# Kernel tuning notes

Measured on AMD Instinct MI355X. Metric: run time of the kernel, lower is better.

The kernel has to match this reference:

```python
import math
import jax, jax.numpy as jnp
import numpy as np

DIM = 256
B, S = 4, 4096

def setup_inputs() -> dict:
    key = jax.random.key(0)
    k1, k2, k3, k4 = jax.random.split(key, 4)
    x = jax.random.normal(k1, (B, S, DIM), dtype=jnp.float32)
    W = jax.random.normal(k2, (3 * DIM, DIM), dtype=jnp.float32) * 0.02
    b = jax.random.normal(k3, (3 * DIM,), dtype=jnp.float32) * 0.02
    attention_mask = jax.random.randint(k4, (B, 1, S), 0, 2, dtype=jnp.int32)
    return {"x": x, "W": W, "b": b, "attention_mask": attention_mask}

def reference(x, W, b, attention_mask):
    # qkv projection: Linear(dim, 3*dim) -> x @ W^T + b
    qkv = jnp.einsum("bsd,ed->bse", x, W) + b  # [B,S,3*DIM]
    q, k, v = jnp.split(qkv, 3, axis=-1)
    # NOTE: module computes q @ v^T (not q @ k^T) -- faithful to source
    scores = jnp.einsum("bqd,bkd->bqk", q, v) / math.sqrt(DIM)  # [B,S,S]
    scores = jnp.where(attention_mask == 0, -jnp.inf, scores)
    attn = jax.nn.softmax(scores, axis=-1)
    # dropout in eval mode -> identity
    out = jnp.einsum("bqk,bkd->bqd", attn, v)  # [B,S,DIM]
    return out
```

## Files before the change

kernel.cpp:

```cpp
#include <hip/hip_runtime.h>
#include <hip/hip_bf16.h>

#define DIMC 256
#define NB 4
#define NS 4096
#define KT 64
#define VS_ELEMS (KT * DIMC)

typedef __attribute__((ext_vector_type(4))) float f32x4;
typedef __attribute__((ext_vector_type(8))) short bf16x8;

__device__ __forceinline__ ushort f2bf(float f) {
  __hip_bfloat16 h = __float2bfloat16(f);
  return *reinterpret_cast<ushort*>(&h);
}
__device__ __forceinline__ float bf2f(ushort h) {
  uint u = ((uint)h) << 16;
  float f;
  __builtin_memcpy(&f, &u, 4);
  return f;
}

__device__ __forceinline__ void gload16(const ushort* g, ushort* l) {
  __builtin_amdgcn_global_load_lds(
      (const __attribute__((address_space(1))) unsigned int*)g,
      (__attribute__((address_space(3))) unsigned int*)l,
      16, 0, 0);
}

__global__ __launch_bounds__(256) void prep_kernel(
    const float* __restrict__ W, const int* __restrict__ mask,
    const float* __restrict__ x,
    ushort* __restrict__ Whl, uint* __restrict__ pm32,
    ushort* __restrict__ xhb, ushort* __restrict__ xlb)
{
  const int bid = blockIdx.x;
  if (bid < 512) {
    const int col = bid;
    const int k = threadIdx.x;
    const int srcrow = (col < 256) ? col : (col + 256);
    float f = W[(size_t)srcrow * 256 + k];
    ushort h = f2bf(f);
    Whl[(size_t)col * 256 + k] = h;
    Whl[131072 + (size_t)col * 256 + k] = f2bf(f - bf2f(h));
  } else if (bid < 514) {
    int t = (bid - 512) * 256 + threadIdx.x;
    int b = t >> 7;
    int kt = (t >> 1) & 63;
    int kh = t & 1;
    const int* mrow = mask + b * NS + kt * 64 + kh * 32;
    uint wd = 0;
    for (int g = 0; g < 4; ++g)
      for (int ntl = 0; ntl < 2; ++ntl)
        for (int r = 0; r < 4; ++r)
          if (mrow[ntl * 16 + 4 * g + r] != 0) wd |= 1u << (8 * g + ntl * 4 + r);
    pm32[t] = wd;
  } else {
    size_t idx = ((size_t)(bid - 514) * 256 + threadIdx.x) * 8;
    float4 f0 = *(const float4*)&x[idx];
    float4 f1 = *(const float4*)&x[idx + 4];
    union { uint4 v; ushort u[8]; } ph, pl;
    #pragma unroll
    for (int e = 0; e < 8; ++e) {
      float fe = (e < 4) ? ((const float*)&f0)[e] : ((const float*)&f1)[e - 4];
      ushort h = f2bf(fe);
      ph.u[e] = h;
      pl.u[e] = f2bf(fe - bf2f(h));
    }
    *(uint4*)&xhb[idx] = ph.v;
    *(uint4*)&xlb[idx] = pl.v;
  }
}

__global__ __launch_bounds__(512) void qv_proj_kernel(
    const ushort* __restrict__ xhb, const ushort* __restrict__ xlb,
    const ushort* __restrict__ Whl, const float* __restrict__ bias,
    ushort* __restrict__ qb, ushort* __restrict__ vb, ushort* __restrict__ vtb)
{
  const int tid  = threadIdx.x;
  const int w    = tid >> 6;
  const int lane = tid & 63;
  const int l15  = lane & 15;
  const int g    = (lane >> 4) & 3;
  const int r0   = blockIdx.x << 6;
  const int colbase = w << 6;

  __shared__ ushort olds[64 * 520];

  f32x4 acc[4][4];
  #pragma unroll
  for (int rt = 0; rt < 4; ++rt)
    #pragma unroll
    for (int ct = 0; ct < 4; ++ct) { acc[rt][ct].x=0.f; acc[rt][ct].y=0.f; acc[rt][ct].z=0.f; acc[rt][ct].w=0.f; }

  #pragma unroll 1
  for (int st = 0; st < 8; ++st) {
    bf16x8 xh[4], xl[4];
    #pragma unroll
    for (int rt = 0; rt < 4; ++rt) {
      const size_t off = (size_t)(r0 + rt * 16 + l15) * DIMC + st * 32 + g * 8;
      xh[rt] = *(const bf16x8*)&xhb[off];
      xl[rt] = *(const bf16x8*)&xlb[off];
    }
    #pragma unroll
    for (int ct = 0; ct < 4; ++ct) {
      const ushort* wp = Whl + (size_t)(colbase + ct * 16 + l15) * 256 + st * 32 + g * 8;
      bf16x8 wh = *(const bf16x8*)wp;
      bf16x8 wl = *(const bf16x8*)(wp + 131072);
      #pragma unroll
      for (int rt = 0; rt < 4; ++rt) {
        acc[rt][ct] = __builtin_amdgcn_mfma_f32_16x16x32_bf16(xh[rt], wh, acc[rt][ct], 0, 0, 0);
        acc[rt][ct] = __builtin_amdgcn_mfma_f32_16x16x32_bf16(xl[rt], wh, acc[rt][ct], 0, 0, 0);
        acc[rt][ct] = __builtin_amdgcn_mfma_f32_16x16x32_bf16(xh[rt], wl, acc[rt][ct], 0, 0, 0);
      }
    }
  }

  const float qscale = (colbase < 256) ? 0.0625f : 1.0f;
  #pragma unroll
  for (int ct = 0; ct < 4; ++ct) {
    const int col = colbase + ct * 16 + l15;
    const float bv = bias[(col < 256) ? col : (col + 256)];
    #pragma unroll
    for (int rt = 0; rt < 4; ++rt) {
      #pragma unroll
      for (int r = 0; r < 4; ++r)
        olds[(rt * 16 + 4 * g + r) * 520 + col] = f2bf((acc[rt][ct][r] + bv) * qscale);
    }
  }
  __syncthreads();

  #pragma unroll
  for (int i = 0; i < 8; ++i) {
    int task = tid + i * 512;
    int row = task >> 6, ch = task & 63;
    uint4 d = *(const uint4*)&olds[row * 520 + ch * 8];
    if (ch < 32) *(uint4*)&qb[(size_t)(r0 + row) * DIMC + ch * 8] = d;
    else         *(uint4*)&vb[(size_t)(r0 + row) * DIMC + (ch - 32) * 8] = d;
  }
  const int bbp = r0 >> 12;
  const int s0  = r0 & (NS - 1);
  const int vcol = tid & 255;
  const int ohalf = (tid >> 8) * 4;
  #pragma unroll
  for (int oo = 0; oo < 4; ++oo) {
    int o = ohalf + oo;
    union { uint4 v; ushort u[8]; } pk;
    #pragma unroll
    for (int j = 0; j < 8; ++j)
      pk.u[j] = olds[(o * 8 + j) * 520 + 256 + vcol];
    *(uint4*)&vtb[((size_t)(bbp * DIMC + vcol)) * NS + s0 + o * 8] = pk.v;
  }
}

__global__ __launch_bounds__(512, 1) void attn_kernel(
    const ushort* __restrict__ qb, const ushort* __restrict__ vb,
    const ushort* __restrict__ vtb, const uint* __restrict__ pm32,
    float* __restrict__ outA, float* __restrict__ opB,
    float* __restrict__ mlA, float* __restrict__ mlB)
{
  const int tid  = threadIdx.x;
  const int w    = tid >> 6;
  const int lane = tid & 63;
  const int l15  = lane & 15;
  const int g    = (lane >> 4) & 3;
  const int kh   = w & 1;
  const int pq   = w >> 1;

  const int s     = blockIdx.x & 1;
  const int qb128 = blockIdx.x >> 1;
  const int qrow0 = qb128 << 7;
  const int bb    = qrow0 >> 12;
  const int koff  = s << 11;

  float* opart = s ? opB : outA;
  float* mlp   = s ? mlB : mlA;

  extern __shared__ __align__(16) char smem[];
  uint*   pmlds = (uint*)smem;
  ushort* vs0  = (ushort*)(smem + 1024);
  ushort* vs1  = vs0 + VS_ELEMS;
  ushort* vt0  = vs1 + VS_ELEMS;
  ushort* vt1  = vt0 + VS_ELEMS;
  ushort* psb  = vt1 + VS_ELEMS;

  bf16x8 qreg[2][8];
  #pragma unroll
  for (int qt = 0; qt < 2; ++qt) {
    const int qrow = qrow0 + (pq << 5) + (qt << 4) + l15;
    #pragma unroll
    for (int st = 0; st < 8; ++st)
      qreg[qt][st] = *(const bf16x8*)&qb[(size_t)qrow * DIMC + ((st * 4 + g) << 3)];
  }

  if (tid < 128) pmlds[tid] = pm32[(bb << 7) + tid];

  auto stage_vs = [&](int kt, ushort* vsN) {
    const ushort* vbase = vb + ((size_t)(bb * NS + koff + kt * KT)) * DIMC;
    #pragma unroll
    for (int i = 0; i < 4; ++i) {
      int rr0 = (w << 3) + (i << 1);
      int row = rr0 + (lane >> 5);
      int cs  = lane & 31;
      gload16(vbase + row * DIMC + ((cs ^ (row & 7)) << 3), vsN + (rr0 << 8));
    }
  };
  auto stage_vt = [&](int kt, ushort* vtN) {
    #pragma unroll
    for (int i = 0; i < 4; ++i) {
      int d0 = i << 6;
      int dim = (d0 + lane) ^ ((w & 3) << 1);
      gload16(vtb + ((size_t)(bb * DIMC + dim)) * NS + koff + kt * KT + (w << 3),
              vtN + ((w << 8) + d0) * 8);
    }
  };

  stage_vs(0, vs0);
  __syncthreads();

  f32x4 acc_o[2][8];
  #pragma unroll
  for (int qt = 0; qt < 2; ++qt)
    #pragma unroll
    for (int nt = 0; nt < 8; ++nt) { acc_o[qt][nt].x=0.f; acc_o[qt][nt].y=0.f; acc_o[qt][nt].z=0.f; acc_o[qt][nt].w=0.f; }
  float l_s[2] = {0.f, 0.f};

  ushort* psw = psb + pq * (32 * 72);

  #pragma unroll 1
  for (int t = 0; t < 32; ++t) {
    ushort* vsQ = (t & 1) ? vs1 : vs0;
    ushort* vsS = (t & 1) ? vs0 : vs1;
    ushort* vtS = (t & 1) ? vt1 : vt0;
    ushort* vtP = (t & 1) ? vt0 : vt1;

    if (t + 1 < 32) stage_vs(t + 1, vsS);
    stage_vt(t, vtS);

    f32x4 sacc[2][2];
    #pragma unroll
    for (int qt = 0; qt < 2; ++qt) {
      sacc[qt][0].x=0.f; sacc[qt][0].y=0.f; sacc[qt][0].z=0.f; sacc[qt][0].w=0.f;
      sacc[qt][1] = sacc[qt][0];
    }
    __builtin_amdgcn_s_setprio(1);
    #pragma unroll
    for (int st = 0; st < 8; ++st) {
      const int key0 = (kh << 5) + l15;
      bf16x8 af0 = *(const bf16x8*)&vsQ[(key0 * 32 + ((st * 4 + g) ^ (key0 & 7))) * 8];
      const int key1 = key0 + 16;
      bf16x8 af1 = *(const bf16x8*)&vsQ[(key1 * 32 + ((st * 4 + g) ^ (key1 & 7))) * 8];
      #pragma unroll
      for (int qt = 0; qt < 2; ++qt) {
        sacc[qt][0] = __builtin_amdgcn_mfma_f32_16x16x32_bf16(af0, qreg[qt][st], sacc[qt][0], 0, 0, 0);
        sacc[qt][1] = __builtin_amdgcn_mfma_f32_16x16x32_bf16(af1, qreg[qt][st], sacc[qt][1], 0, 0, 0);
      }
    }
    __builtin_amdgcn_s_setprio(0);

    if (t > 0) {
      bf16x8 pa[2][2];
      #pragma unroll
      for (int qt = 0; qt < 2; ++qt)
        #pragma unroll
        for (int ks2 = 0; ks2 < 2; ++ks2)
          pa[qt][ks2] = *(const bf16x8*)&psw[((qt << 4) + l15) * 72 + (ks2 << 5) + (g << 3)];
      __builtin_amdgcn_s_setprio(1);
      #pragma unroll
      for (int ntl = 0; ntl < 8; ++ntl) {
        const int d = ((kh << 3) + ntl) * 16 + l15;
        #pragma unroll
        for (int ks2 = 0; ks2 < 2; ++ks2) {
          const int kc = (ks2 << 2) + g;
          bf16x8 vf = *(const bf16x8*)&vtP[((kc << 8) + (d ^ ((kc & 3) << 1))) * 8];
          acc_o[0][ntl] = __builtin_amdgcn_mfma_f32_16x16x32_bf16(vf, pa[0][ks2], acc_o[0][ntl], 0, 0, 0);
          acc_o[1][ntl] = __builtin_amdgcn_mfma_f32_16x16x32_bf16(vf, pa[1][ks2], acc_o[1][ntl], 0, 0, 0);
        }
      }
      __builtin_amdgcn_s_setprio(0);
    }

    const int ktg = (s << 5) + t;
    uint mybits = (pmlds[(ktg << 1) + kh] >> (g << 3)) & 0xffu;
    float pv[2][8];
    #pragma unroll
    for (int qt = 0; qt < 2; ++qt) {
      #pragma unroll
      for (int ntl = 0; ntl < 2; ++ntl)
        #pragma unroll
        for (int r = 0; r < 4; ++r) {
          float vv = (mybits & (1u << (ntl * 4 + r))) ? sacc[qt][ntl][r] : -1e30f;
          pv[qt][ntl * 4 + r] = __expf(vv);
        }
      float rs = ((pv[qt][0] + pv[qt][1]) + (pv[qt][2] + pv[qt][3])) +
                 ((pv[qt][4] + pv[qt][5]) + (pv[qt][6] + pv[qt][7]));
      rs += __shfl_xor(rs, 16);
      rs += __shfl_xor(rs, 32);
      l_s[qt] += rs;
    }

    asm volatile("s_waitcnt lgkmcnt(0)" ::: "memory");
    __builtin_amdgcn_sched_barrier(0);
    __builtin_amdgcn_s_barrier();
    __builtin_amdgcn_sched_barrier(0);

    #pragma unroll
    for (int qt = 0; qt < 2; ++qt) {
      #pragma unroll
      for (int ntl = 0; ntl < 2; ++ntl) {
        uint2 pk;
        pk.x = (uint)f2bf(pv[qt][ntl*4+0]) | ((uint)f2bf(pv[qt][ntl*4+1]) << 16);
        pk.y = (uint)f2bf(pv[qt][ntl*4+2]) | ((uint)f2bf(pv[qt][ntl*4+3]) << 16);
        *(uint2*)&psw[((qt << 4) + l15) * 72 + (kh << 5) + ntl * 16 + 4 * g] = pk;
      }
    }

    if (t + 1 < 32)
      asm volatile("s_waitcnt vmcnt(8) lgkmcnt(0)" ::: "memory");
    else
      asm volatile("s_waitcnt vmcnt(4) lgkmcnt(0)" ::: "memory");
    __builtin_amdgcn_sched_barrier(0);
    __builtin_amdgcn_s_barrier();
    __builtin_amdgcn_sched_barrier(0);
  }

  asm volatile("s_waitcnt vmcnt(0)" ::: "memory");
  __builtin_amdgcn_sched_barrier(0);
  __builtin_amdgcn_s_barrier();
  __builtin_amdgcn_sched_barrier(0);
  {
    ushort* vtP = vt1;
    bf16x8 pa[2][2];
    #pragma unroll
    for (int qt = 0; qt < 2; ++qt)
      #pragma unroll
      for (int ks2 = 0; ks2 < 2; ++ks2)
        pa[qt][ks2] = *(const bf16x8*)&psw[((qt << 4) + l15) * 72 + (ks2 << 5) + (g << 3)];
    __builtin_amdgcn_s_setprio(1);
    #pragma unroll
    for (int ntl = 0; ntl < 8; ++ntl) {
      const int d = ((kh << 3) + ntl) * 16 + l15;
      #pragma unroll
      for (int ks2 = 0; ks2 < 2; ++ks2) {
        const int kc = (ks2 << 2) + g;
        bf16x8 vf = *(const bf16x8*)&vtP[((kc << 8) + (d ^ ((kc & 3) << 1))) * 8];
        acc_o[0][ntl] = __builtin_amdgcn_mfma_f32_16x16x32_bf16(vf, pa[0][ks2], acc_o[0][ntl], 0, 0, 0);
        acc_o[1][ntl] = __builtin_amdgcn_mfma_f32_16x16x32_bf16(vf, pa[1][ks2], acc_o[1][ntl], 0, 0, 0);
      }
    }
    __builtin_amdgcn_s_setprio(0);
  }

  #pragma unroll
  for (int qt = 0; qt < 2; ++qt) {
    const int qrow = qrow0 + (pq << 5) + (qt << 4) + l15;
    const size_t obase = (size_t)qrow * DIMC + 4 * g;
    #pragma unroll
    for (int ntl = 0; ntl < 8; ++ntl) {
      f32x4 o = acc_o[qt][ntl];
      *(float4*)&opart[obase + ((kh << 3) + ntl) * 16] = *(float4*)&o;
    }
    if (g == 0) mlp[(size_t)qrow * 2 + kh] = l_s[qt];
  }
}

__global__ __launch_bounds__(256) void merge_kernel(
    float* __restrict__ outA, const float* __restrict__ opB,
    const float* __restrict__ mlA, const float* __restrict__ mlB)
{
  int id = blockIdx.x * 256 + threadIdx.x;
  int row = id >> 6;
  int c = (id & 63) << 2;
  float lT = (mlA[(size_t)row * 2] + mlA[(size_t)row * 2 + 1]) +
             (mlB[(size_t)row * 2] + mlB[(size_t)row * 2 + 1]);
  float inv = 1.f / lT;
  size_t o = (size_t)row * DIMC + c;
  float4 a = *(const float4*)&outA[o];
  float4 b = *(const float4*)&opB[o];
  float4 r;
  r.x = (a.x + b.x) * inv;
  r.y = (a.y + b.y) * inv;
  r.z = (a.z + b.z) * inv;
  r.w = (a.w + b.w) * inv;
  *(float4*)&outA[o] = r;
}

extern "C" void kernel_launch(void* const* d_in, const int* in_sizes, int n_in,
                              void* d_out, int out_size, void* d_ws, size_t ws_size,
                              hipStream_t stream) {
  const float* x    = (const float*)d_in[0];
  const float* W    = (const float*)d_in[1];
  const float* bias = (const float*)d_in[2];
  const int*   mask = (const int*)d_in[3];
  float* out = (float*)d_out;

  const size_t n = (size_t)NB * NS * DIMC;
  ushort* qb  = (ushort*)d_ws;
  ushort* vb  = qb + n;
  ushort* vtb = vb + n;
  uint* pm32 = (uint*)(vtb + n);
  ushort* Whl = (ushort*)(pm32 + 512);
  float* opB = (float*)(Whl + 262144);
  float* mlA = opB + n;
  float* mlB = mlA + 2 * (NB * NS);
  ushort* xhb = (ushort*)opB;
  ushort* xlb = xhb + n;

  prep_kernel<<<2562, 256, 0, stream>>>(W, mask, x, Whl, pm32, xhb, xlb);
  qv_proj_kernel<<<(NB * NS) / 64, 512, 0, stream>>>(xhb, xlb, Whl, bias, qb, vb, vtb);

  const int smem_bytes = 1024 + 4 * VS_ELEMS * 2 + 4 * 32 * 72 * 2;
  attn_kernel<<<256, 512, smem_bytes, stream>>>(qb, vb, vtb, pm32, out, opB, mlA, mlB);
  merge_kernel<<<(NB * NS * DIMC / 4) / 256, 256, 0, stream>>>(out, opB, mlA, mlB);
}
```

Measured before the change: 147.4 us.

## Double attention block to 1024 threads, splitting key and output tiles over four waves

The attention kernel now launches 1024 threads per block instead of 512. Each 128-query tile is covered by four key-quarter waves rather than two, so each wave handles 16 keys of the score tile and 64 output dims of the PV product. Staging loads, the mask-bit extraction, the P-tile layout and the row-sum partials are all remapped, and the merge kernel now adds four partial sums per split. The aim is more waves per CU to hide latency and to cut per-wave register pressure. The cost is duplicated Q registers and pa LDS reads across more waves, plus barrier cost at 1024 threads.

```diff
diff --git a/kernel.cpp b/kernel.cpp
--- a/kernel.cpp
+++ b/kernel.cpp
@@ -153,7 +153,7 @@
   }
 }
 
-__global__ __launch_bounds__(512, 1) void attn_kernel(
+__global__ __launch_bounds__(1024, 1) void attn_kernel(
     const ushort* __restrict__ qb, const ushort* __restrict__ vb,
     const ushort* __restrict__ vtb, const uint* __restrict__ pm32,
     float* __restrict__ outA, float* __restrict__ opB,
@@ -164,8 +164,8 @@
   const int lane = tid & 63;
   const int l15  = lane & 15;
   const int g    = (lane >> 4) & 3;
-  const int kh   = w & 1;
-  const int pq   = w >> 1;
+  const int kh   = w & 3;
+  const int pq   = w >> 2;
 
   const int s     = blockIdx.x & 1;
   const int qb128 = blockIdx.x >> 1;
@@ -198,31 +198,32 @@
   auto stage_vs = [&](int kt, ushort* vsN) {
     const ushort* vbase = vb + ((size_t)(bb * NS + koff + kt * KT)) * DIMC;
     #pragma unroll
-    for (int i = 0; i < 4; ++i) {
-      int rr0 = (w << 3) + (i << 1);
+    for (int i = 0; i < 2; ++i) {
+      int rr0 = (w << 2) + (i << 1);
       int row = rr0 + (lane >> 5);
       int cs  = lane & 31;
       gload16(vbase + row * DIMC + ((cs ^ (row & 7)) << 3), vsN + (rr0 << 8));
     }
   };
   auto stage_vt = [&](int kt, ushort* vtN) {
-    #pragma unroll
-    for (int i = 0; i < 4; ++i) {
-      int d0 = i << 6;
-      int dim = (d0 + lane) ^ ((w & 3) << 1);
-      gload16(vtb + ((size_t)(bb * DIMC + dim)) * NS + koff + kt * KT + (w << 3),
-              vtN + ((w << 8) + d0) * 8);
+    const int kc = w >> 1;
+    #pragma unroll
+    for (int i = 0; i < 2; ++i) {
+      int d0 = ((w & 1) << 7) + (i << 6);
+      int dim = (d0 + lane) ^ ((kc & 3) << 1);
+      gload16(vtb + ((size_t)(bb * DIMC + dim)) * NS + koff + kt * KT + (kc << 3),
+              vtN + ((kc << 8) + d0) * 8);
     }
   };
 
   stage_vs(0, vs0);
   __syncthreads();
 
-  f32x4 acc_o[2][8];
+  f32x4 acc_o[2][4];
   #pragma unroll
   for (int qt = 0; qt < 2; ++qt)
     #pragma unroll
-    for (int nt = 0; nt < 8; ++nt) { acc_o[qt][nt].x=0.f; acc_o[qt][nt].y=0.f; acc_o[qt][nt].z=0.f; acc_o[qt][nt].w=0.f; }
+    for (int nt = 0; nt < 4; ++nt) { acc_o[qt][nt].x=0.f; acc_o[qt][nt].y=0.f; acc_o[qt][nt].z=0.f; acc_o[qt][nt].w=0.f; }
   float l_s[2] = {0.f, 0.f};
 
   ushort* psw = psb + pq * (32 * 72);
@@ -237,24 +238,16 @@
     if (t + 1 < 32) stage_vs(t + 1, vsS);
     stage_vt(t, vtS);
 
-    f32x4 sacc[2][2];
-    #pragma unroll
-    for (int qt = 0; qt < 2; ++qt) {
-      sacc[qt][0].x=0.f; sacc[qt][0].y=0.f; sacc[qt][0].z=0.f; sacc[qt][0].w=0.f;
-      sacc[qt][1] = sacc[qt][0];
-    }
+    f32x4 sacc[2];
+    sacc[0].x=0.f; sacc[0].y=0.f; sacc[0].z=0.f; sacc[0].w=0.f;
+    sacc[1] = sacc[0];
     __builtin_amdgcn_s_setprio(1);
     #pragma unroll
     for (int st = 0; st < 8; ++st) {
-      const int key0 = (kh << 5) + l15;
-      bf16x8 af0 = *(const bf16x8*)&vsQ[(key0 * 32 + ((st * 4 + g) ^ (key0 & 7))) * 8];
-      const int key1 = key0 + 16;
-      bf16x8 af1 = *(const bf16x8*)&vsQ[(key1 * 32 + ((st * 4 + g) ^ (key1 & 7))) * 8];
-      #pragma unroll
-      for (int qt = 0; qt < 2; ++qt) {
-        sacc[qt][0] = __builtin_amdgcn_mfma_f32_16x16x32_bf16(af0, qreg[qt][st], sacc[qt][0], 0, 0, 0);
-        sacc[qt][1] = __builtin_amdgcn_mfma_f32_16x16x32_bf16(af1, qreg[qt][st], sacc[qt][1], 0, 0, 0);
-      }
+      const int key = (kh << 4) + l15;
+      bf16x8 af = *(const bf16x8*)&vsQ[(key * 32 + ((st * 4 + g) ^ (key & 7))) * 8];
+      sacc[0] = __builtin_amdgcn_mfma_f32_16x16x32_bf16(af, qreg[0][st], sacc[0], 0, 0, 0);
+      sacc[1] = __builtin_amdgcn_mfma_f32_16x16x32_bf16(af, qreg[1][st], sacc[1], 0, 0, 0);
     }
     __builtin_amdgcn_s_setprio(0);
 
@@ -267,8 +260,8 @@
           pa[qt][ks2] = *(const bf16x8*)&psw[((qt << 4) + l15) * 72 + (ks2 << 5) + (g << 3)];
       __builtin_amdgcn_s_setprio(1);
       #pragma unroll
-      for (int ntl = 0; ntl < 8; ++ntl) {
-        const int d = ((kh << 3) + ntl) * 16 + l15;
+      for (int ntl = 0; ntl < 4; ++ntl) {
+        const int d = ((kh << 2) + ntl) * 16 + l15;
         #pragma unroll
         for (int ks2 = 0; ks2 < 2; ++ks2) {
           const int kc = (ks2 << 2) + g;
@@ -281,19 +274,16 @@
     }
 
     const int ktg = (s << 5) + t;
-    uint mybits = (pmlds[(ktg << 1) + kh] >> (g << 3)) & 0xffu;
-    float pv[2][8];
+    uint mybits = (pmlds[(ktg << 1) + (kh >> 1)] >> ((g << 3) + ((kh & 1) << 2))) & 0xfu;
+    float pv[2][4];
     #pragma unroll
     for (int qt = 0; qt < 2; ++qt) {
       #pragma unroll
-      for (int ntl = 0; ntl < 2; ++ntl)
-        #pragma unroll
-        for (int r = 0; r < 4; ++r) {
-          float vv = (mybits & (1u << (ntl * 4 + r))) ? sacc[qt][ntl][r] : -1e30f;
-          pv[qt][ntl * 4 + r] = __expf(vv);
-        }
-      float rs = ((pv[qt][0] + pv[qt][1]) + (pv[qt][2] + pv[qt][3])) +
-                 ((pv[qt][4] + pv[qt][5]) + (pv[qt][6] + pv[qt][7]));
+      for (int r = 0; r < 4; ++r) {
+        float vv = (mybits & (1u << r)) ? sacc[qt][r] : -1e30f;
+        pv[qt][r] = __expf(vv);
+      }
+      float rs = (pv[qt][0] + pv[qt][1]) + (pv[qt][2] + pv[qt][3]);
       rs += __shfl_xor(rs, 16);
       rs += __shfl_xor(rs, 32);
       l_s[qt] += rs;
@@ -306,19 +296,16 @@
 
     #pragma unroll
     for (int qt = 0; qt < 2; ++qt) {
-      #pragma unroll
-      for (int ntl = 0; ntl < 2; ++ntl) {
-        uint2 pk;
-        pk.x = (uint)f2bf(pv[qt][ntl*4+0]) | ((uint)f2bf(pv[qt][ntl*4+1]) << 16);
-        pk.y = (uint)f2bf(pv[qt][ntl*4+2]) | ((uint)f2bf(pv[qt][ntl*4+3]) << 16);
-        *(uint2*)&psw[((qt << 4) + l15) * 72 + (kh << 5) + ntl * 16 + 4 * g] = pk;
-      }
+      uint2 pk;
+      pk.x = (uint)f2bf(pv[qt][0]) | ((uint)f2bf(pv[qt][1]) << 16);
+      pk.y = (uint)f2bf(pv[qt][2]) | ((uint)f2bf(pv[qt][3]) << 16);
+      *(uint2*)&psw[((qt << 4) + l15) * 72 + (kh << 4) + (g << 2)] = pk;
     }
 
     if (t + 1 < 32)
-      asm volatile("s_waitcnt vmcnt(8) lgkmcnt(0)" ::: "memory");
+      asm volatile("s_waitcnt vmcnt(4) lgkmcnt(0)" ::: "memory");
     else
-      asm volatile("s_waitcnt vmcnt(4) lgkmcnt(0)" ::: "memory");
+      asm volatile("s_waitcnt vmcnt(2) lgkmcnt(0)" ::: "memory");
     __builtin_amdgcn_sched_barrier(0);
     __builtin_amdgcn_s_barrier();
     __builtin_amdgcn_sched_barrier(0);
@@ -338,8 +325,8 @@
         pa[qt][ks2] = *(const bf16x8*)&psw[((qt << 4) + l15) * 72 + (ks2 << 5) + (g << 3)];
     __builtin_amdgcn_s_setprio(1);
     #pragma unroll
-    for (int ntl = 0; ntl < 8; ++ntl) {
-      const int d = ((kh << 3) + ntl) * 16 + l15;
+    for (int ntl = 0; ntl < 4; ++ntl) {
+      const int d = ((kh << 2) + ntl) * 16 + l15;
       #pragma unroll
       for (int ks2 = 0; ks2 < 2; ++ks2) {
         const int kc = (ks2 << 2) + g;
@@ -356,11 +343,11 @@
     const int qrow = qrow0 + (pq << 5) + (qt << 4) + l15;
     const size_t obase = (size_t)qrow * DIMC + 4 * g;
     #pragma unroll
-    for (int ntl = 0; ntl < 8; ++ntl) {
+    for (int ntl = 0; ntl < 4; ++ntl) {
       f32x4 o = acc_o[qt][ntl];
-      *(float4*)&opart[obase + ((kh << 3) + ntl) * 16] = *(float4*)&o;
-    }
-    if (g == 0) mlp[(size_t)qrow * 2 + kh] = l_s[qt];
+      *(float4*)&opart[obase + ((kh << 2) + ntl) * 16] = *(float4*)&o;
+    }
+    if (g == 0) mlp[(size_t)qrow * 4 + kh] = l_s[qt];
   }
 }
 
@@ -371,8 +358,10 @@
   int id = blockIdx.x * 256 + threadIdx.x;
   int row = id >> 6;
   int c = (id & 63) << 2;
-  float lT = (mlA[(size_t)row * 2] + mlA[(size_t)row * 2 + 1]) +
-             (mlB[(size_t)row * 2] + mlB[(size_t)row * 2 + 1]);
+  float lT = ((mlA[(size_t)row * 4] + mlA[(size_t)row * 4 + 1]) +
+              (mlA[(size_t)row * 4 + 2] + mlA[(size_t)row * 4 + 3])) +
+             ((mlB[(size_t)row * 4] + mlB[(size_t)row * 4 + 1]) +
+              (mlB[(size_t)row * 4 + 2] + mlB[(size_t)row * 4 + 3]));
   float inv = 1.f / lT;
   size_t o = (size_t)row * DIMC + c;
   float4 a = *(const float4*)&outA[o];
@@ -402,7 +391,7 @@
   ushort* Whl = (ushort*)(pm32 + 512);
   float* opB = (float*)(Whl + 262144);
   float* mlA = opB + n;
-  float* mlB = mlA + 2 * (NB * NS);
+  float* mlB = mlA + 4 * (NB * NS);
   ushort* xhb = (ushort*)opB;
   ushort* xlb = xhb + n;
 
@@ -410,6 +399,6 @@
   qv_proj_kernel<<<(NB * NS) / 64, 512, 0, stream>>>(xhb, xlb, Whl, bias, qb, vb, vtb);
 
   const int smem_bytes = 1024 + 4 * VS_ELEMS * 2 + 4 * 32 * 72 * 2;
-  attn_kernel<<<256, 512, smem_bytes, stream>>>(qb, vb, vtb, pm32, out, opB, mlA, mlB);
+  attn_kernel<<<256, 1024, smem_bytes, stream>>>(qb, vb, vtb, pm32, out, opB, mlA, mlB);
   merge_kernel<<<(NB * NS * DIMC / 4) / 256, 256, 0, stream>>>(out, opB, mlA, mlB);
 }
```

Measured after the change: 335.0 us. 2.27x slower.

## Fuse split-K merge into attention kernel via last-block atomic counter

Applied to the files above, without the earlier changes.

Drops the separate merge kernel. Each pair of split-K attention blocks for the same query tile increments an atomic counter after writing its partial output and row sums. The second block to finish reads the other block's partial, adds its own register accumulators, normalizes and writes the final output. This removes one launch and one full read/write pass over the output, at the cost of a fence, an atomic and a serialized tail in the last block of each pair.

```diff
diff --git a/kernel.cpp b/kernel.cpp
--- a/kernel.cpp
+++ b/kernel.cpp
@@ -32,7 +32,8 @@
     const float* __restrict__ W, const int* __restrict__ mask,
     const float* __restrict__ x,
     ushort* __restrict__ Whl, uint* __restrict__ pm32,
-    ushort* __restrict__ xhb, ushort* __restrict__ xlb)
+    ushort* __restrict__ xhb, ushort* __restrict__ xlb,
+    uint* __restrict__ flags)
 {
   const int bid = blockIdx.x;
   if (bid < 512) {
@@ -55,6 +56,7 @@
         for (int r = 0; r < 4; ++r)
           if (mrow[ntl * 16 + 4 * g + r] != 0) wd |= 1u << (8 * g + ntl * 4 + r);
     pm32[t] = wd;
+    if (bid == 512 && threadIdx.x < 128) flags[threadIdx.x] = 0;
   } else {
     size_t idx = ((size_t)(bid - 514) * 256 + threadIdx.x) * 8;
     float4 f0 = *(const float4*)&x[idx];
@@ -157,7 +159,8 @@
     const ushort* __restrict__ qb, const ushort* __restrict__ vb,
     const ushort* __restrict__ vtb, const uint* __restrict__ pm32,
     float* __restrict__ outA, float* __restrict__ opB,
-    float* __restrict__ mlA, float* __restrict__ mlB)
+    float* __restrict__ mlA, float* __restrict__ mlB,
+    uint* __restrict__ flags)
 {
   const int tid  = threadIdx.x;
   const int w    = tid >> 6;
@@ -178,6 +181,7 @@
 
   extern __shared__ __align__(16) char smem[];
   uint*   pmlds = (uint*)smem;
+  uint*   lastf = (uint*)(smem + 512);
   ushort* vs0  = (ushort*)(smem + 1024);
   ushort* vs1  = vs0 + VS_ELEMS;
   ushort* vt0  = vs1 + VS_ELEMS;
@@ -362,27 +366,37 @@
     }
     if (g == 0) mlp[(size_t)qrow * 2 + kh] = l_s[qt];
   }
-}
-
-__global__ __launch_bounds__(256) void merge_kernel(
-    float* __restrict__ outA, const float* __restrict__ opB,
-    const float* __restrict__ mlA, const float* __restrict__ mlB)
-{
-  int id = blockIdx.x * 256 + threadIdx.x;
-  int row = id >> 6;
-  int c = (id & 63) << 2;
-  float lT = (mlA[(size_t)row * 2] + mlA[(size_t)row * 2 + 1]) +
-             (mlB[(size_t)row * 2] + mlB[(size_t)row * 2 + 1]);
-  float inv = 1.f / lT;
-  size_t o = (size_t)row * DIMC + c;
-  float4 a = *(const float4*)&outA[o];
-  float4 b = *(const float4*)&opB[o];
-  float4 r;
-  r.x = (a.x + b.x) * inv;
-  r.y = (a.y + b.y) * inv;
-  r.z = (a.z + b.z) * inv;
-  r.w = (a.w + b.w) * inv;
-  *(float4*)&outA[o] = r;
+
+  asm volatile("s_waitcnt vmcnt(0)" ::: "memory");
+  __syncthreads();
+  if (tid == 0) {
+    __threadfence();
+    lastf[0] = atomicAdd(&flags[qb128], 1u);
+  }
+  __syncthreads();
+  if (lastf[0] == 1) {
+    __threadfence();
+    const float* po = s ? outA : opB;
+    #pragma unroll
+    for (int qt = 0; qt < 2; ++qt) {
+      const int qrow = qrow0 + (pq << 5) + (qt << 4) + l15;
+      float lT = (mlA[(size_t)qrow * 2] + mlA[(size_t)qrow * 2 + 1]) +
+                 (mlB[(size_t)qrow * 2] + mlB[(size_t)qrow * 2 + 1]);
+      float inv = 1.f / lT;
+      const size_t obase = (size_t)qrow * DIMC + 4 * g;
+      #pragma unroll
+      for (int ntl = 0; ntl < 8; ++ntl) {
+        const size_t off = obase + ((kh << 3) + ntl) * 16;
+        float4 p = *(const float4*)&po[off];
+        f32x4 o;
+        o.x = (acc_o[qt][ntl].x + p.x) * inv;
+        o.y = (acc_o[qt][ntl].y + p.y) * inv;
+        o.z = (acc_o[qt][ntl].z + p.z) * inv;
+        o.w = (acc_o[qt][ntl].w + p.w) * inv;
+        *(float4*)&outA[off] = *(float4*)&o;
+      }
+    }
+  }
 }
 
 extern "C" void kernel_launch(void* const* d_in, const int* in_sizes, int n_in,
@@ -403,13 +417,13 @@
   float* opB = (float*)(Whl + 262144);
   float* mlA = opB + n;
   float* mlB = mlA + 2 * (NB * NS);
+  uint* flags = (uint*)(mlB + 2 * (NB * NS));
   ushort* xhb = (ushort*)opB;
   ushort* xlb = xhb + n;
 
-  prep_kernel<<<2562, 256, 0, stream>>>(W, mask, x, Whl, pm32, xhb, xlb);
+  prep_kernel<<<2562, 256, 0, stream>>>(W, mask, x, Whl, pm32, xhb, xlb, flags);
   qv_proj_kernel<<<(NB * NS) / 64, 512, 0, stream>>>(xhb, xlb, Whl, bias, qb, vb, vtb);
 
   const int smem_bytes = 1024 + 4 * VS_ELEMS * 2 + 4 * 32 * 72 * 2;
-  attn_kernel<<<256, 512, smem_bytes, stream>>>(qb, vb, vtb, pm32, out, opB, mlA, mlB);
-  merge_kernel<<<(NB * NS * DIMC / 4) / 256, 256, 0, stream>>>(out, opB, mlA, mlB);
-}
+  attn_kernel<<<256, 512, smem_bytes, stream>>>(qb, vb, vtb, pm32, out, opB, mlA, mlB, flags);
+}
```

After: 178.3 us. 21.0% more time.
